# Performance work log

Measured on AMD Instinct MI355X. Metric: run time of the kernel, lower is better.

Reference implementation:

```python
import jax, jax.numpy as jnp
import numpy as np
import math

N_HEADS = 16
N_POINTS = 4
EPS = 1e-6


def layer_norm(x, g, b):
    m = x.mean(-1, keepdims=True)
    v = ((x - m) ** 2).mean(-1, keepdims=True)
    return (x - m) / jnp.sqrt(v + EPS) * g + b


def ref_points(H, W, dtype):
    # matches CrossSelfAtt.get_reference_points for one square level -> (1, H*W, 1, 2) in (x, y)
    ys = (jnp.arange(H, dtype=dtype) + 0.5) / H
    xs = (jnp.arange(W, dtype=dtype) + 0.5) / W
    gy, gx = jnp.meshgrid(ys, xs, indexing='ij')
    return jnp.stack([gx.reshape(-1), gy.reshape(-1)], -1)[None, :, None, :]


def bilinear(v, H, W, loc):
    # v: (B, H*W, nH, Dh); loc: (B, Lq, nH, P, 2) normalized [0,1]; zero padding, align_corners=False
    B, _, nH, Dh = v.shape
    Lq, P = loc.shape[1], loc.shape[3]
    x = loc[..., 0] * W - 0.5
    y = loc[..., 1] * H - 0.5
    x0 = jnp.floor(x)
    y0 = jnp.floor(y)
    wx1 = x - x0
    wy1 = y - y0
    x0i = x0.astype(jnp.int32)
    y0i = y0.astype(jnp.int32)
    vt = v.transpose(0, 2, 1, 3)  # (B, nH, HW, Dh)

    def corner(xi, yi, w):
        valid = (xi >= 0) & (xi < W) & (yi >= 0) & (yi < H)
        idx = jnp.clip(yi, 0, H - 1) * W + jnp.clip(xi, 0, W - 1)  # (B, Lq, nH, P)
        idx_t = idx.transpose(0, 2, 1, 3).reshape(B, nH, Lq * P)
        g = jnp.take_along_axis(vt, idx_t[..., None], axis=2).reshape(B, nH, Lq, P, Dh)
        return g.transpose(0, 2, 1, 3, 4) * (w * valid)[..., None]

    return (corner(x0i, y0i, (1 - wx1) * (1 - wy1))
            + corner(x0i + 1, y0i, wx1 * (1 - wy1))
            + corner(x0i, y0i + 1, (1 - wx1) * wy1)
            + corner(x0i + 1, y0i + 1, wx1 * wy1))


def msda(query, value_in, shapes, ref, Wv, bv, Woff, boff, Wa, ba, Wo, bo):
    # standard Deformable-DETR MSDeformAttn forward
    B, Lq, D = query.shape
    nH, P, L = N_HEADS, N_POINTS, len(shapes)
    Dh = D // nH
    value = (value_in @ Wv + bv).reshape(B, -1, nH, Dh)
    off = (query @ Woff + boff).reshape(B, Lq, nH, L, P, 2)
    aw = jax.nn.softmax((query @ Wa + ba).reshape(B, Lq, nH, L * P), -1).reshape(B, Lq, nH, L, P)
    norm = jnp.asarray([[w_, h_] for (h_, w_) in shapes], dtype=query.dtype)  # (L, 2) = (W, H)
    loc = ref[:, :, None, :, None, :] + off / norm[None, None, None, :, None, :]
    out = jnp.zeros((B, Lq, nH, Dh), query.dtype)
    start = 0
    for l, (H_, W_) in enumerate(shapes):
        samp = bilinear(value[:, start:start + H_ * W_], H_, W_, loc[:, :, :, l])
        out = out + (samp * aw[:, :, :, l, :, None]).sum(3)
        start += H_ * W_
    return out.reshape(B, Lq, D) @ Wo + bo


def setup_inputs() -> dict:
    key = jax.random.key(0)
    B, Lq, Lf, D = 2, 4096, 4096, 768
    nH, P, L = N_HEADS, N_POINTS, 1
    ks = jax.random.split(key, 20)
    w = lambda k, s: jax.random.normal(k, s, jnp.float32) * 0.02
    return {
        'query': jax.random.normal(ks[0], (B, Lq, D), jnp.float32),
        'feat': jax.random.normal(ks[1], (B, Lf, D), jnp.float32),
        'spatial_shapes': jnp.array([[64, 64]], jnp.int32),
        'level_start_index': jnp.array([0], jnp.int32),
        'qn_W': w(ks[2], (D, D)), 'qn_b': jnp.zeros((D,)), 'qn_g': jnp.ones((D,)), 'qn_beta': jnp.zeros((D,)),
        'fn_W': w(ks[3], (D, D)), 'fn_b': jnp.zeros((D,)), 'fn_g': jnp.ones((D,)), 'fn_beta': jnp.zeros((D,)),
        'nm_g': jnp.ones((D,)), 'nm_beta': jnp.zeros((D,)),
        'gamma1': jax.random.normal(ks[4], (D,), jnp.float32) * 0.1,
        'c_Wv': w(ks[5], (D, D)), 'c_bv': jnp.zeros((D,)),
        'c_Woff': w(ks[6], (D, nH * L * P * 2)),
        'c_boff': jax.random.uniform(ks[7], (nH * L * P * 2,), jnp.float32, -3.0, 3.0),
        'c_Wa': w(ks[8], (D, nH * L * P)), 'c_ba': jnp.zeros((nH * L * P,)),
        'c_Wo': w(ks[9], (D, D)), 'c_bo': jnp.zeros((D,)),
        's_Wv': w(ks[10], (D, D)), 's_bv': jnp.zeros((D,)),
        's_Woff': w(ks[11], (D, nH * L * P * 2)),
        's_boff': jax.random.uniform(ks[12], (nH * L * P * 2,), jnp.float32, -3.0, 3.0),
        's_Wa': w(ks[13], (D, nH * L * P)), 's_ba': jnp.zeros((nH * L * P,)),
        's_Wo': w(ks[14], (D, D)), 's_bo': jnp.zeros((D,)),
    }


def reference(query, feat, spatial_shapes, level_start_index, qn_W, qn_b, qn_g, qn_beta, fn_W, fn_b, fn_g, fn_beta, nm_g, nm_beta, gamma1, c_Wv, c_bv, c_Woff, c_boff, c_Wa, c_ba, c_Wo, c_bo, s_Wv, s_bv, s_Woff, s_boff, s_Wa, s_ba, s_Wo, s_bo):
    shapes = [(int(h), int(w_)) for h, w_ in np.asarray(spatial_shapes)]
    qe = int(math.sqrt(query.shape[1]))
    ref = ref_points(qe, qe, query.dtype)  # (1, Lq, 1, 2)
    qn = layer_norm(query @ qn_W + qn_b, qn_g, qn_beta)
    fn = layer_norm(feat @ fn_W + fn_b, fn_g, fn_beta)
    attn = msda(qn, fn, shapes, ref, c_Wv, c_bv, c_Woff, c_boff, c_Wa, c_ba, c_Wo, c_bo)
    attn1 = layer_norm(attn, nm_g, nm_beta)
    attn2 = msda(attn1, attn1, [(qe, qe)], ref, s_Wv, s_bv, s_Woff, s_boff, s_Wa, s_ba, s_Wo, s_bo)
    # note: source uses gamma1 for BOTH terms (gamma2 is unused)
    return attn * gamma1 + attn2 * gamma1
```

## Files before the change

kernel.cpp:

```cpp
#include <hip/hip_runtime.h>
#include <hip/hip_bf16.h>
#include <math.h>

#define D_MODEL 768
#define NH 16
#define DH 48
#define NP 4
#define LQ 4096
#define BB 2
#define MTOT (BB * LQ)

typedef __attribute__((ext_vector_type(8))) _Float16 half8_t;
typedef __attribute__((ext_vector_type(4))) float floatx4;

__device__ __forceinline__ void load_lds16(const void* g, void* l) {
    __builtin_amdgcn_global_load_lds((const __attribute__((address_space(1))) void*)g,
                                     (__attribute__((address_space(3))) void*)l, 16, 0, 0);
}

template <int MODE>
__device__ __forceinline__ void gemm_body(
    const _Float16* __restrict__ A, const _Float16* __restrict__ Wt,
    const float* __restrict__ bias, void* __restrict__ Cv, int ldc,
    int tm, int tn,
    const _Float16* __restrict__ attn, const float* __restrict__ gamma)
{
    constexpr int K = 768;
    constexpr int NT = K / 32;
    __shared__ _Float16 As[2][128 * 32];
    __shared__ _Float16 Bs[2][128 * 32];

    const int bm = tm * 128, bn = tn * 128;
    const int t = threadIdx.x;
    const int lane = t & 63;
    const int w = t >> 6;
    const int wm = (w >> 1) * 64, wn = (w & 1) * 64;

    floatx4 acc[4][4] = {};

    const int r0 = t >> 2;
    const int c8 = (t & 3) * 8;
    const size_t arow0 = (size_t)(bm + r0) * K + c8;
    const size_t arow1 = (size_t)(bm + 64 + r0) * K + c8;
    const size_t brow0 = (size_t)(bn + r0) * K + c8;
    const size_t brow1 = (size_t)(bn + 64 + r0) * K + c8;

    const int lrow = lane & 15;
    const int lk = (lane >> 4) * 8;

    load_lds16(A + arow0, &As[0][w * 512]);
    load_lds16(A + arow1, &As[0][2048 + w * 512]);
    load_lds16(Wt + brow0, &Bs[0][w * 512]);
    load_lds16(Wt + brow1, &Bs[0][2048 + w * 512]);
    __syncthreads();

    for (int ti = 0; ti < NT; ++ti) {
        const int cur = ti & 1;
        if (ti + 1 < NT) {
            const int kn = (ti + 1) * 32;
            const int nxt = cur ^ 1;
            load_lds16(A + arow0 + kn, &As[nxt][w * 512]);
            load_lds16(A + arow1 + kn, &As[nxt][2048 + w * 512]);
            load_lds16(Wt + brow0 + kn, &Bs[nxt][w * 512]);
            load_lds16(Wt + brow1 + kn, &Bs[nxt][2048 + w * 512]);
        }

        const _Float16* Ac = As[cur];
        const _Float16* Bc = Bs[cur];
        half8_t af[4], bf[4];
#pragma unroll
        for (int i = 0; i < 4; ++i) {
            af[i] = *(const half8_t*)&Ac[(wm + i * 16 + lrow) * 32 + lk];
            bf[i] = *(const half8_t*)&Bc[(wn + i * 16 + lrow) * 32 + lk];
        }
#pragma unroll
        for (int i = 0; i < 4; ++i)
#pragma unroll
            for (int j = 0; j < 4; ++j)
                acc[i][j] = __builtin_amdgcn_mfma_f32_16x16x32_f16(af[i], bf[j], acc[i][j], 0, 0, 0);

        if (ti + 1 < NT) __syncthreads();
    }

    const int rquad = (lane >> 4) * 4;
#pragma unroll
    for (int i = 0; i < 4; ++i) {
#pragma unroll
        for (int j = 0; j < 4; ++j) {
            const int col = bn + wn + j * 16 + lrow;
            const float bcol = bias[col];
#pragma unroll
            for (int r = 0; r < 4; ++r) {
                const size_t row = (size_t)(bm + wm + i * 16 + rquad + r);
                float v = acc[i][j][r] + bcol;
                if constexpr (MODE == 1) {
                    v = ((float)attn[row * (size_t)ldc + col] + v) * gamma[col];
                    ((float*)Cv)[row * (size_t)ldc + col] = v;
                } else if constexpr (MODE == 2) {
                    ((_Float16*)Cv)[row * (size_t)ldc + col] = (_Float16)v;
                } else {
                    ((float*)Cv)[row * (size_t)ldc + col] = v;
                }
            }
        }
    }
}

template <int MODE>
__global__ __launch_bounds__(256) void gemm_mfma(
    const _Float16* __restrict__ A, const _Float16* __restrict__ Wt,
    const float* __restrict__ bias, void* __restrict__ C,
    const _Float16* __restrict__ attn, const float* __restrict__ gamma)
{
    const int bid = blockIdx.x;
    const int swz = (bid & 7) * 48 + (bid >> 3);
    gemm_body<MODE>(A, Wt, bias, C, 768, swz & 63, swz >> 6, attn, gamma);
}

template <int M0, int M1>
__global__ __launch_bounds__(256) void dual_gemm(
    const _Float16* __restrict__ A0, const _Float16* __restrict__ W0,
    const float* __restrict__ b0, void* __restrict__ C0, int ldc0, int cnt0,
    const _Float16* __restrict__ A1, const _Float16* __restrict__ W1,
    const float* __restrict__ b1, void* __restrict__ C1, int ldc1, int cnt1)
{
    int bid = blockIdx.x;
    if (bid < cnt0) {
        const int q = cnt0 >> 3;
        const int swz = (bid & 7) * q + (bid >> 3);
        gemm_body<M0>(A0, W0, b0, C0, ldc0, swz & 63, swz >> 6, nullptr, nullptr);
    } else {
        bid -= cnt0;
        const int q = cnt1 >> 3;
        const int swz = (bid & 7) * q + (bid >> 3);
        gemm_body<M1>(A1, W1, b1, C1, ldc1, swz & 63, swz >> 6, nullptr, nullptr);
    }
}

__device__ __forceinline__ void ln_wave_body(
    const _Float16* __restrict__ X, _Float16* __restrict__ A,
    const float* __restrict__ g, const float* __restrict__ beta, int row)
{
    const int lane = threadIdx.x & 63;
    const _Float16* x = X + (size_t)row * D_MODEL;
    float v[12];
    float s = 0.f, s2 = 0.f;
#pragma unroll
    for (int j = 0; j < 12; ++j) {
        v[j] = (float)x[lane + 64 * j];
        s += v[j];
        s2 += v[j] * v[j];
    }
#pragma unroll
    for (int m = 1; m < 64; m <<= 1) {
        s += __shfl_xor(s, m);
        s2 += __shfl_xor(s2, m);
    }
    const float mean = s * (1.f / 768.f);
    const float var = s2 * (1.f / 768.f) - mean * mean;
    const float rstd = rsqrtf(var + 1e-6f);
    _Float16* arow = A + (size_t)row * D_MODEL;
#pragma unroll
    for (int j = 0; j < 12; ++j) {
        const int cc = lane + 64 * j;
        arow[cc] = (_Float16)((v[j] - mean) * rstd * g[cc] + beta[cc]);
    }
}

__global__ __launch_bounds__(256) void ln2_wave(
    const _Float16* __restrict__ X0, _Float16* __restrict__ A0,
    const float* __restrict__ g0, const float* __restrict__ b0,
    const _Float16* __restrict__ X1, _Float16* __restrict__ A1,
    const float* __restrict__ g1, const float* __restrict__ b1)
{
    const int r = blockIdx.x * 4 + (threadIdx.x >> 6);
    if (r < MTOT) ln_wave_body(X0, A0, g0, b0, r);
    else          ln_wave_body(X1, A1, g1, b1, r - MTOT);
}

__global__ __launch_bounds__(256) void ln_wave(
    const _Float16* __restrict__ X, _Float16* __restrict__ A,
    const float* __restrict__ g, const float* __restrict__ beta)
{
    const int r = blockIdx.x * 4 + (threadIdx.x >> 6);
    ln_wave_body(X, A, g, beta, r);
}

__global__ __launch_bounds__(256) void convert_all(
    const float* __restrict__ query, _Float16* __restrict__ actA,
    const float* __restrict__ feat, _Float16* __restrict__ actB,
    const float* __restrict__ w0, const float* __restrict__ w1,
    const float* __restrict__ w2, const float* __restrict__ w3,
    const float* __restrict__ w4, const float* __restrict__ w5,
    _Float16* __restrict__ Wall,
    const float* __restrict__ Woff_c, const float* __restrict__ Wa_c,
    const float* __restrict__ boff_c, const float* __restrict__ ba_c,
    const float* __restrict__ Woff_s, const float* __restrict__ Wa_s,
    const float* __restrict__ boff_s, const float* __restrict__ ba_s,
    _Float16* __restrict__ Wc, _Float16* __restrict__ Ws,
    float* __restrict__ bias_c, float* __restrict__ bias_s)
{
    __shared__ float tile[32][33];
    const int bid = blockIdx.x;
    const int t = threadIdx.x;

    if (bid < 12288) {
        const int i = bid * 256 + t;
        const int sel = i / (MTOT * 192);
        const int r = i - sel * (MTOT * 192);
        const float* X = sel ? feat : query;
        _Float16* D = sel ? actB : actA;
        const int c4 = r * 4;
        const float4 v = *(const float4*)(X + (size_t)c4);
        _Float16 o[4] = {(_Float16)v.x, (_Float16)v.y, (_Float16)v.z, (_Float16)v.w};
        *(uint2*)(D + (size_t)c4) = *(uint2*)o;
    } else if (bid < 15744) {
        const int g = bid - 12288;
        const int wi = g / 576;
        const int gx = g - wi * 576;
        const float* W = (wi == 0) ? w0 : (wi == 1) ? w1 : (wi == 2) ? w2
                       : (wi == 3) ? w3 : (wi == 4) ? w4 : w5;
        _Float16* Wt = Wall + (size_t)wi * 768 * 768;
        const int tk0 = (gx / 24) * 32;
        const int tn0 = (gx % 24) * 32;
#pragma unroll
        for (int r = 0; r < 4; ++r) {
            const int row = r * 8 + (t >> 5);
            const int col = t & 31;
            tile[row][col] = W[(size_t)(tk0 + row) * 768 + tn0 + col];
        }
        __syncthreads();
        const int n = t >> 3;
        const int kq = (t & 7) * 4;
        _Float16* dst = Wt + (size_t)(tn0 + n) * 768 + tk0 + kq;
#pragma unroll
        for (int u = 0; u < 4; ++u) dst[u] = (_Float16)tile[kq + u][n];
    } else {
        const int i = (bid - 15744) * 256 + t;
        if (i >= 2 * 256 * 192) return;
        const int pair = i / (256 * 192);
        const int r = i - pair * (256 * 192);
        const int n = r / 192;
        const int k0 = (r - n * 192) * 4;
        const float* Woff = pair ? Woff_s : Woff_c;
        const float* Wa = pair ? Wa_s : Wa_c;
        _Float16* dst = pair ? Ws : Wc;
        _Float16* row = dst + (size_t)n * 768;
#pragma unroll
        for (int u = 0; u < 4; ++u) {
            const int k = k0 + u;
            float v = (n < 128) ? Woff[(size_t)k * 128 + n]
                    : (n < 192) ? Wa[(size_t)k * 64 + (n - 128)] : 0.f;
            row[k] = (_Float16)v;
        }
        if (k0 == 0) {
            const float* boff = pair ? boff_s : boff_c;
            const float* ba = pair ? ba_s : ba_c;
            float* bias = pair ? bias_s : bias_c;
            bias[n] = (n < 128) ? boff[n] : (n < 192) ? ba[n - 128] : 0.f;
        }
    }
}

__global__ __launch_bounds__(192) void sample_fused(
    const _Float16* __restrict__ value, const float* __restrict__ offc,
    _Float16* __restrict__ A)
{
    __shared__ float loc_s[32][8];
    __shared__ float aw_s[32][4];

    const int bid = blockIdx.x;
    const int swz = (bid & 7) * 512 + (bid >> 3);
    const int bq_base = swz * 2;
    const int t = threadIdx.x;

    if (t < 32) {
        const int bq = bq_base + (t >> 4);
        const int h = t & 15;
        const int q = bq & (LQ - 1);
        const float* orow = offc + (size_t)bq * 256 + h * 8;
        const float* arow = offc + (size_t)bq * 256 + 128 + h * 4;
        float a0 = arow[0], a1 = arow[1], a2 = arow[2], a3 = arow[3];
        float mx = fmaxf(fmaxf(a0, a1), fmaxf(a2, a3));
        float e0 = expf(a0 - mx), e1 = expf(a1 - mx), e2 = expf(a2 - mx), e3 = expf(a3 - mx);
        float r = 1.f / (e0 + e1 + e2 + e3);
        const float refx = ((q & 63) + 0.5f) * (1.f / 64.f);
        const float refy = ((q >> 6) + 0.5f) * (1.f / 64.f);
#pragma unroll
        for (int p = 0; p < 4; ++p) {
            loc_s[t][p * 2 + 0] = refx + orow[p * 2 + 0] * (1.f / 64.f);
            loc_s[t][p * 2 + 1] = refy + orow[p * 2 + 1] * (1.f / 64.f);
        }
        aw_s[t][0] = e0 * r; aw_s[t][1] = e1 * r;
        aw_s[t][2] = e2 * r; aw_s[t][3] = e3 * r;
    }
    __syncthreads();

    const int lbqh = t / 6;
    const int c = t - lbqh * 6;
    const int d0 = c * 8;
    const int bq = bq_base + (lbqh >> 4);
    const int h = lbqh & 15;
    const int b = bq >> 12;

    const _Float16* vbase = value + (size_t)b * LQ * D_MODEL + h * DH + d0;

    float acc[8] = {};
#pragma unroll
    for (int p = 0; p < 4; ++p) {
        const float x = loc_s[lbqh][p * 2 + 0] * 64.f - 0.5f;
        const float y = loc_s[lbqh][p * 2 + 1] * 64.f - 0.5f;
        const float xf = floorf(x), yf = floorf(y);
        const float wx1 = x - xf, wy1 = y - yf;
        const float wx0 = 1.f - wx1, wy0 = 1.f - wy1;
        const int x0 = (int)xf, y0 = (int)yf;
        const int x1 = x0 + 1, y1 = y0 + 1;
        const float wp = aw_s[lbqh][p];
        const bool vx0 = (x0 >= 0) && (x0 < 64);
        const bool vx1 = (x1 >= 0) && (x1 < 64);
        const bool vy0 = (y0 >= 0) && (y0 < 64);
        const bool vy1 = (y1 >= 0) && (y1 < 64);
        const float cw[4] = {wp * wx0 * wy0, wp * wx1 * wy0, wp * wx0 * wy1, wp * wx1 * wy1};
        const bool cv[4] = {vx0 && vy0, vx1 && vy0, vx0 && vy1, vx1 && vy1};
        const int cxy[4][2] = {{x0, y0}, {x1, y0}, {x0, y1}, {x1, y1}};
#pragma unroll
        for (int k = 0; k < 4; ++k) {
            if (cv[k]) {
                const half8_t g = *(const half8_t*)(vbase + (size_t)(cxy[k][1] * 64 + cxy[k][0]) * D_MODEL);
#pragma unroll
                for (int u = 0; u < 8; ++u) acc[u] += cw[k] * (float)g[u];
            }
        }
    }

    _Float16* arow = A + (size_t)bq * D_MODEL + h * DH + d0;
    _Float16 o[8];
#pragma unroll
    for (int u = 0; u < 8; ++u) o[u] = (_Float16)acc[u];
    *(uint4*)arow = *(uint4*)o;
}

extern "C" void kernel_launch(void* const* d_in, const int* in_sizes, int n_in,
                              void* d_out, int out_size, void* d_ws, size_t ws_size,
                              hipStream_t stream)
{
    const float* query   = (const float*)d_in[0];
    const float* feat    = (const float*)d_in[1];
    const float* qn_W    = (const float*)d_in[4];
    const float* qn_b    = (const float*)d_in[5];
    const float* qn_g    = (const float*)d_in[6];
    const float* qn_beta = (const float*)d_in[7];
    const float* fn_W    = (const float*)d_in[8];
    const float* fn_b    = (const float*)d_in[9];
    const float* fn_g    = (const float*)d_in[10];
    const float* fn_beta = (const float*)d_in[11];
    const float* nm_g    = (const float*)d_in[12];
    const float* nm_beta = (const float*)d_in[13];
    const float* gamma1  = (const float*)d_in[14];
    const float* c_Wv    = (const float*)d_in[15];
    const float* c_bv    = (const float*)d_in[16];
    const float* c_Woff  = (const float*)d_in[17];
    const float* c_boff  = (const float*)d_in[18];
    const float* c_Wa    = (const float*)d_in[19];
    const float* c_ba    = (const float*)d_in[20];
    const float* c_Wo    = (const float*)d_in[21];
    const float* c_bo    = (const float*)d_in[22];
    const float* s_Wv    = (const float*)d_in[23];
    const float* s_bv    = (const float*)d_in[24];
    const float* s_Woff  = (const float*)d_in[25];
    const float* s_boff  = (const float*)d_in[26];
    const float* s_Wa    = (const float*)d_in[27];
    const float* s_ba    = (const float*)d_in[28];
    const float* s_Wo    = (const float*)d_in[29];
    const float* s_bo    = (const float*)d_in[30];

    const size_t SZ = (size_t)MTOT * D_MODEL;
    _Float16* hA    = (_Float16*)d_ws;
    _Float16* hB    = hA + SZ;
    _Float16* hQ    = hB + SZ;
    _Float16* hF    = hQ + SZ;
    _Float16* val16 = hF + SZ;
    float* offc   = (float*)(val16 + SZ);
    float* bias_c = offc + (size_t)MTOT * 256;
    float* bias_s = bias_c + 256;
    _Float16* W6 = (_Float16*)(bias_s + 256);
    _Float16* W_qn  = W6 + (size_t)0 * 768 * 768;
    _Float16* W_fn  = W6 + (size_t)1 * 768 * 768;
    _Float16* W_cWv = W6 + (size_t)2 * 768 * 768;
    _Float16* W_cWo = W6 + (size_t)3 * 768 * 768;
    _Float16* W_sWv = W6 + (size_t)4 * 768 * 768;
    _Float16* W_sWo = W6 + (size_t)5 * 768 * 768;
    _Float16* Woffa_c = W6 + (size_t)6 * 768 * 768;
    _Float16* Woffa_s = Woffa_c + (size_t)256 * 768;

    float* out = (float*)d_out;
    const dim3 blk(256);

    convert_all<<<16128, blk, 0, stream>>>(
        query, hA, feat, hB,
        qn_W, fn_W, c_Wv, c_Wo, s_Wv, s_Wo, W6,
        c_Woff, c_Wa, c_boff, c_ba, s_Woff, s_Wa, s_boff, s_ba,
        Woffa_c, Woffa_s, bias_c, bias_s);

    dual_gemm<2, 2><<<768, blk, 0, stream>>>(hA, W_qn, qn_b, hQ, 768, 384,
                                             hB, W_fn, fn_b, hF, 768, 384);
    ln2_wave<<<2 * MTOT / 4, blk, 0, stream>>>(hQ, hQ, qn_g, qn_beta,
                                               hF, hF, fn_g, fn_beta);
    dual_gemm<2, 0><<<512, blk, 0, stream>>>(hF, W_cWv, c_bv, val16, 768, 384,
                                             hQ, Woffa_c, bias_c, offc, 256, 128);
    sample_fused<<<4096, dim3(192), 0, stream>>>(val16, offc, hB);
    gemm_mfma<2><<<384, blk, 0, stream>>>(hB, W_cWo, c_bo, hA, nullptr, nullptr);

    ln_wave<<<MTOT / 4, blk, 0, stream>>>(hA, hQ, nm_g, nm_beta);
    dual_gemm<2, 0><<<512, blk, 0, stream>>>(hQ, W_sWv, s_bv, val16, 768, 384,
                                             hQ, Woffa_s, bias_s, offc, 256, 128);
    sample_fused<<<4096, dim3(192), 0, stream>>>(val16, offc, hB);
    gemm_mfma<1><<<384, blk, 0, stream>>>(hB, W_sWo, s_bo, out, hA, gamma1);
}
```

Baseline: 346.2 us.

## Fuse fp32 activation conversion into first GEMMs and store offsets as fp16

The first projection GEMMs now read fp32 query/feat directly, converting to fp16 in registers before the LDS store. This removes the separate activation conversion pass and its extra round trip through memory. The remaining weight transposes and these GEMMs are merged into one mega launch, with only the qn/fn weight transposes split into their own small kernel beforehand. The offset and attention-logit buffer is now fp16 instead of fp32, which halves that traffic at some cost in precision for the sampling locations. The fp32 A path uses register staging with a full vmcnt wait instead of async LDS loads, so loads may overlap less with compute.

Result: slower. 365.4 us (+5.5%).

```diff
diff --git a/kernel.cpp b/kernel.cpp
--- a/kernel.cpp
+++ b/kernel.cpp
@@ -18,9 +18,9 @@
                                      (__attribute__((address_space(3))) void*)l, 16, 0, 0);
 }
 
-template <int MODE>
+template <int MODE, bool AFP32>
 __device__ __forceinline__ void gemm_body(
-    const _Float16* __restrict__ A, const _Float16* __restrict__ Wt,
+    const void* __restrict__ Av, const _Float16* __restrict__ Wt,
     const float* __restrict__ bias, void* __restrict__ Cv, int ldc,
     int tm, int tn,
     const _Float16* __restrict__ attn, const float* __restrict__ gamma)
@@ -40,29 +40,60 @@
 
     const int r0 = t >> 2;
     const int c8 = (t & 3) * 8;
+    const size_t brow0 = (size_t)(bn + r0) * K + c8;
+    const size_t brow1 = (size_t)(bn + 64 + r0) * K + c8;
+
+    const int lrow = lane & 15;
+    const int lk = (lane >> 4) * 8;
+
+    const _Float16* A16 = (const _Float16*)Av;
+    const float* A32 = (const float*)Av;
     const size_t arow0 = (size_t)(bm + r0) * K + c8;
     const size_t arow1 = (size_t)(bm + 64 + r0) * K + c8;
-    const size_t brow0 = (size_t)(bn + r0) * K + c8;
-    const size_t brow1 = (size_t)(bn + 64 + r0) * K + c8;
-
-    const int lrow = lane & 15;
-    const int lk = (lane >> 4) * 8;
-
-    load_lds16(A + arow0, &As[0][w * 512]);
-    load_lds16(A + arow1, &As[0][2048 + w * 512]);
-    load_lds16(Wt + brow0, &Bs[0][w * 512]);
-    load_lds16(Wt + brow1, &Bs[0][2048 + w * 512]);
+
+    float4 ar[4];
+
+    auto STAGE_B = [&](int kt, int buf) {
+        load_lds16(Wt + brow0 + kt, &Bs[buf][w * 512]);
+        load_lds16(Wt + brow1 + kt, &Bs[buf][2048 + w * 512]);
+    };
+    auto STAGE_A16 = [&](int kt, int buf) {
+        load_lds16(A16 + arow0 + kt, &As[buf][w * 512]);
+        load_lds16(A16 + arow1 + kt, &As[buf][2048 + w * 512]);
+    };
+    auto LOAD_A32 = [&](int kt) {
+        const float* p0 = A32 + arow0 + kt;
+        const float* p1 = A32 + arow1 + kt;
+        ar[0] = *(const float4*)p0; ar[1] = *(const float4*)(p0 + 4);
+        ar[2] = *(const float4*)p1; ar[3] = *(const float4*)(p1 + 4);
+    };
+    auto WRITE_A32 = [&](int buf) {
+        _Float16 h0[8] = {(_Float16)ar[0].x, (_Float16)ar[0].y, (_Float16)ar[0].z, (_Float16)ar[0].w,
+                          (_Float16)ar[1].x, (_Float16)ar[1].y, (_Float16)ar[1].z, (_Float16)ar[1].w};
+        _Float16 h1[8] = {(_Float16)ar[2].x, (_Float16)ar[2].y, (_Float16)ar[2].z, (_Float16)ar[2].w,
+                          (_Float16)ar[3].x, (_Float16)ar[3].y, (_Float16)ar[3].z, (_Float16)ar[3].w};
+        *(half8_t*)&As[buf][r0 * 32 + c8] = *(half8_t*)h0;
+        *(half8_t*)&As[buf][2048 + r0 * 32 + c8] = *(half8_t*)h1;
+    };
+
+    STAGE_B(0, 0);
+    if constexpr (AFP32) {
+        LOAD_A32(0);
+        asm volatile("s_waitcnt vmcnt(0)" ::: "memory");
+        WRITE_A32(0);
+    } else {
+        STAGE_A16(0, 0);
+    }
     __syncthreads();
 
     for (int ti = 0; ti < NT; ++ti) {
         const int cur = ti & 1;
+        const int nxt = cur ^ 1;
         if (ti + 1 < NT) {
             const int kn = (ti + 1) * 32;
-            const int nxt = cur ^ 1;
-            load_lds16(A + arow0 + kn, &As[nxt][w * 512]);
-            load_lds16(A + arow1 + kn, &As[nxt][2048 + w * 512]);
-            load_lds16(Wt + brow0 + kn, &Bs[nxt][w * 512]);
-            load_lds16(Wt + brow1 + kn, &Bs[nxt][2048 + w * 512]);
+            STAGE_B(kn, nxt);
+            if constexpr (AFP32) LOAD_A32(kn);
+            else                 STAGE_A16(kn, nxt);
         }
 
         const _Float16* Ac = As[cur];
@@ -79,7 +110,13 @@
             for (int j = 0; j < 4; ++j)
                 acc[i][j] = __builtin_amdgcn_mfma_f32_16x16x32_f16(af[i], bf[j], acc[i][j], 0, 0, 0);
 
-        if (ti + 1 < NT) __syncthreads();
+        if (ti + 1 < NT) {
+            if constexpr (AFP32) {
+                asm volatile("s_waitcnt vmcnt(0)" ::: "memory");
+                WRITE_A32(nxt);
+            }
+            __syncthreads();
+        }
     }
 
     const int rquad = (lane >> 4) * 4;
@@ -96,100 +133,49 @@
                 if constexpr (MODE == 1) {
                     v = ((float)attn[row * (size_t)ldc + col] + v) * gamma[col];
                     ((float*)Cv)[row * (size_t)ldc + col] = v;
-                } else if constexpr (MODE == 2) {
+                } else {
                     ((_Float16*)Cv)[row * (size_t)ldc + col] = (_Float16)v;
-                } else {
-                    ((float*)Cv)[row * (size_t)ldc + col] = v;
                 }
             }
         }
     }
 }
 
-template <int MODE>
-__global__ __launch_bounds__(256) void gemm_mfma(
-    const _Float16* __restrict__ A, const _Float16* __restrict__ Wt,
-    const float* __restrict__ bias, void* __restrict__ C,
-    const _Float16* __restrict__ attn, const float* __restrict__ gamma)
-{
-    const int bid = blockIdx.x;
-    const int swz = (bid & 7) * 48 + (bid >> 3);
-    gemm_body<MODE>(A, Wt, bias, C, 768, swz & 63, swz >> 6, attn, gamma);
-}
-
-template <int M0, int M1>
-__global__ __launch_bounds__(256) void dual_gemm(
-    const _Float16* __restrict__ A0, const _Float16* __restrict__ W0,
-    const float* __restrict__ b0, void* __restrict__ C0, int ldc0, int cnt0,
-    const _Float16* __restrict__ A1, const _Float16* __restrict__ W1,
-    const float* __restrict__ b1, void* __restrict__ C1, int ldc1, int cnt1)
-{
-    int bid = blockIdx.x;
-    if (bid < cnt0) {
-        const int q = cnt0 >> 3;
-        const int swz = (bid & 7) * q + (bid >> 3);
-        gemm_body<M0>(A0, W0, b0, C0, ldc0, swz & 63, swz >> 6, nullptr, nullptr);
-    } else {
-        bid -= cnt0;
-        const int q = cnt1 >> 3;
-        const int swz = (bid & 7) * q + (bid >> 3);
-        gemm_body<M1>(A1, W1, b1, C1, ldc1, swz & 63, swz >> 6, nullptr, nullptr);
-    }
-}
-
-__device__ __forceinline__ void ln_wave_body(
-    const _Float16* __restrict__ X, _Float16* __restrict__ A,
-    const float* __restrict__ g, const float* __restrict__ beta, int row)
-{
-    const int lane = threadIdx.x & 63;
-    const _Float16* x = X + (size_t)row * D_MODEL;
-    float v[12];
-    float s = 0.f, s2 = 0.f;
-#pragma unroll
-    for (int j = 0; j < 12; ++j) {
-        v[j] = (float)x[lane + 64 * j];
-        s += v[j];
-        s2 += v[j] * v[j];
-    }
-#pragma unroll
-    for (int m = 1; m < 64; m <<= 1) {
-        s += __shfl_xor(s, m);
-        s2 += __shfl_xor(s2, m);
-    }
-    const float mean = s * (1.f / 768.f);
-    const float var = s2 * (1.f / 768.f) - mean * mean;
-    const float rstd = rsqrtf(var + 1e-6f);
-    _Float16* arow = A + (size_t)row * D_MODEL;
-#pragma unroll
-    for (int j = 0; j < 12; ++j) {
-        const int cc = lane + 64 * j;
-        arow[cc] = (_Float16)((v[j] - mean) * rstd * g[cc] + beta[cc]);
-    }
-}
-
-__global__ __launch_bounds__(256) void ln2_wave(
-    const _Float16* __restrict__ X0, _Float16* __restrict__ A0,
-    const float* __restrict__ g0, const float* __restrict__ b0,
-    const _Float16* __restrict__ X1, _Float16* __restrict__ A1,
-    const float* __restrict__ g1, const float* __restrict__ b1)
-{
-    const int r = blockIdx.x * 4 + (threadIdx.x >> 6);
-    if (r < MTOT) ln_wave_body(X0, A0, g0, b0, r);
-    else          ln_wave_body(X1, A1, g1, b1, r - MTOT);
-}
-
-__global__ __launch_bounds__(256) void ln_wave(
-    const _Float16* __restrict__ X, _Float16* __restrict__ A,
-    const float* __restrict__ g, const float* __restrict__ beta)
-{
-    const int r = blockIdx.x * 4 + (threadIdx.x >> 6);
-    ln_wave_body(X, A, g, beta, r);
-}
-
-__global__ __launch_bounds__(256) void convert_all(
-    const float* __restrict__ query, _Float16* __restrict__ actA,
-    const float* __restrict__ feat, _Float16* __restrict__ actB,
+__device__ __forceinline__ void wt_transpose_block(
+    const float* __restrict__ W, _Float16* __restrict__ Wt, int gx, int t,
+    float (*tile)[33])
+{
+    const int tk0 = (gx / 24) * 32;
+    const int tn0 = (gx % 24) * 32;
+#pragma unroll
+    for (int r = 0; r < 4; ++r) {
+        const int row = r * 8 + (t >> 5);
+        const int col = t & 31;
+        tile[row][col] = W[(size_t)(tk0 + row) * 768 + tn0 + col];
+    }
+    __syncthreads();
+    const int n = t >> 3;
+    const int kq = (t & 7) * 4;
+    _Float16* dst = Wt + (size_t)(tn0 + n) * 768 + tk0 + kq;
+#pragma unroll
+    for (int u = 0; u < 4; ++u) dst[u] = (_Float16)tile[kq + u][n];
+}
+
+__global__ __launch_bounds__(256) void convert_w2(
     const float* __restrict__ w0, const float* __restrict__ w1,
+    _Float16* __restrict__ Wall)
+{
+    __shared__ float tile[32][33];
+    const int wi = blockIdx.x / 576;
+    const int gx = blockIdx.x % 576;
+    wt_transpose_block(wi ? w1 : w0, Wall + (size_t)wi * 768 * 768, gx, threadIdx.x, tile);
+}
+
+__global__ __launch_bounds__(256) void g1_mega(
+    const float* __restrict__ query, const _Float16* __restrict__ Wq,
+    const float* __restrict__ bq_, _Float16* __restrict__ Cq,
+    const float* __restrict__ feat, const _Float16* __restrict__ Wf,
+    const float* __restrict__ bf_, _Float16* __restrict__ Cf,
     const float* __restrict__ w2, const float* __restrict__ w3,
     const float* __restrict__ w4, const float* __restrict__ w5,
     _Float16* __restrict__ Wall,
@@ -204,40 +190,21 @@
     const int bid = blockIdx.x;
     const int t = threadIdx.x;
 
-    if (bid < 12288) {
-        const int i = bid * 256 + t;
-        const int sel = i / (MTOT * 192);
-        const int r = i - sel * (MTOT * 192);
-        const float* X = sel ? feat : query;
-        _Float16* D = sel ? actB : actA;
-        const int c4 = r * 4;
-        const float4 v = *(const float4*)(X + (size_t)c4);
-        _Float16 o[4] = {(_Float16)v.x, (_Float16)v.y, (_Float16)v.z, (_Float16)v.w};
-        *(uint2*)(D + (size_t)c4) = *(uint2*)o;
-    } else if (bid < 15744) {
-        const int g = bid - 12288;
+    if (bid < 768) {
+        int b = (bid < 384) ? bid : bid - 384;
+        const int swz = (b & 7) * 48 + (b >> 3);
+        if (bid < 384)
+            gemm_body<2, true>(query, Wq, bq_, Cq, 768, swz & 63, swz >> 6, nullptr, nullptr);
+        else
+            gemm_body<2, true>(feat, Wf, bf_, Cf, 768, swz & 63, swz >> 6, nullptr, nullptr);
+    } else if (bid < 3072) {
+        const int g = bid - 768;
         const int wi = g / 576;
         const int gx = g - wi * 576;
-        const float* W = (wi == 0) ? w0 : (wi == 1) ? w1 : (wi == 2) ? w2
-                       : (wi == 3) ? w3 : (wi == 4) ? w4 : w5;
-        _Float16* Wt = Wall + (size_t)wi * 768 * 768;
-        const int tk0 = (gx / 24) * 32;
-        const int tn0 = (gx % 24) * 32;
-#pragma unroll
-        for (int r = 0; r < 4; ++r) {
-            const int row = r * 8 + (t >> 5);
-            const int col = t & 31;
-            tile[row][col] = W[(size_t)(tk0 + row) * 768 + tn0 + col];
-        }
-        __syncthreads();
-        const int n = t >> 3;
-        const int kq = (t & 7) * 4;
-        _Float16* dst = Wt + (size_t)(tn0 + n) * 768 + tk0 + kq;
-#pragma unroll
-        for (int u = 0; u < 4; ++u) dst[u] = (_Float16)tile[kq + u][n];
+        const float* W = (wi == 0) ? w2 : (wi == 1) ? w3 : (wi == 2) ? w4 : w5;
+        wt_transpose_block(W, Wall + (size_t)(wi + 2) * 768 * 768, gx, t, tile);
     } else {
-        const int i = (bid - 15744) * 256 + t;
-        if (i >= 2 * 256 * 192) return;
+        const int i = (bid - 3072) * 256 + t;
         const int pair = i / (256 * 192);
         const int r = i - pair * (256 * 192);
         const int n = r / 192;
@@ -262,8 +229,87 @@
     }
 }
 
+template <int MODE>
+__global__ __launch_bounds__(256) void gemm_mfma(
+    const _Float16* __restrict__ A, const _Float16* __restrict__ Wt,
+    const float* __restrict__ bias, void* __restrict__ C,
+    const _Float16* __restrict__ attn, const float* __restrict__ gamma)
+{
+    const int bid = blockIdx.x;
+    const int swz = (bid & 7) * 48 + (bid >> 3);
+    gemm_body<MODE, false>(A, Wt, bias, C, 768, swz & 63, swz >> 6, attn, gamma);
+}
+
+__global__ __launch_bounds__(256) void dual_gemm(
+    const _Float16* __restrict__ A0, const _Float16* __restrict__ W0,
+    const float* __restrict__ b0, void* __restrict__ C0, int ldc0, int cnt0,
+    const _Float16* __restrict__ A1, const _Float16* __restrict__ W1,
+    const float* __restrict__ b1, void* __restrict__ C1, int ldc1, int cnt1)
+{
+    int bid = blockIdx.x;
+    if (bid < cnt0) {
+        const int q = cnt0 >> 3;
+        const int swz = (bid & 7) * q + (bid >> 3);
+        gemm_body<2, false>(A0, W0, b0, C0, ldc0, swz & 63, swz >> 6, nullptr, nullptr);
+    } else {
+        bid -= cnt0;
+        const int q = cnt1 >> 3;
+        const int swz = (bid & 7) * q + (bid >> 3);
+        gemm_body<2, false>(A1, W1, b1, C1, ldc1, swz & 63, swz >> 6, nullptr, nullptr);
+    }
+}
+
+__device__ __forceinline__ void ln_wave_body(
+    const _Float16* __restrict__ X, _Float16* __restrict__ A,
+    const float* __restrict__ g, const float* __restrict__ beta, int row)
+{
+    const int lane = threadIdx.x & 63;
+    const _Float16* x = X + (size_t)row * D_MODEL;
+    float v[12];
+    float s = 0.f, s2 = 0.f;
+#pragma unroll
+    for (int j = 0; j < 12; ++j) {
+        v[j] = (float)x[lane + 64 * j];
+        s += v[j];
+        s2 += v[j] * v[j];
+    }
+#pragma unroll
+    for (int m = 1; m < 64; m <<= 1) {
+        s += __shfl_xor(s, m);
+        s2 += __shfl_xor(s2, m);
+    }
+    const float mean = s * (1.f / 768.f);
+    const float var = s2 * (1.f / 768.f) - mean * mean;
+    const float rstd = rsqrtf(var + 1e-6f);
+    _Float16* arow = A + (size_t)row * D_MODEL;
+#pragma unroll
+    for (int j = 0; j < 12; ++j) {
+        const int cc = lane + 64 * j;
+        arow[cc] = (_Float16)((v[j] - mean) * rstd * g[cc] + beta[cc]);
+    }
+}
+
+__global__ __launch_bounds__(256) void ln2_wave(
+    const _Float16* __restrict__ X0, _Float16* __restrict__ A0,
+    const float* __restrict__ g0, const float* __restrict__ b0,
+    const _Float16* __restrict__ X1, _Float16* __restrict__ A1,
+    const float* __restrict__ g1, const float* __restrict__ b1)
+{
+    const int r = blockIdx.x * 4 + (threadIdx.x >> 6);
+    if (r < MTOT) ln_wave_body(X0, A0, g0, b0, r);
+    else          ln_wave_body(X1, A1, g1, b1, r - MTOT);
+}
+
+__global__ __launch_bounds__(256) void ln_wave(
+    const _Float16* __restrict__ X, _Float16* __restrict__ A,
+    const float* __restrict__ g, const float* __restrict__ beta)
+{
+    const int r = blockIdx.x * 4 + (threadIdx.x >> 6);
+    ln_wave_body(X, A, g, beta, r);
+}
+
 __global__ __launch_bounds__(192) void sample_fused(
-    const _Float16* __restrict__ value, const float* __restrict__ offc,
+    const _Float16* __restrict__ value, const _Float16* __restrict__ offc,
     _Float16* __restrict__ A)
 {
     __shared__ float loc_s[32][8];
@@ -278,9 +324,9 @@
         const int bq = bq_base + (t >> 4);
         const int h = t & 15;
         const int q = bq & (LQ - 1);
-        const float* orow = offc + (size_t)bq * 256 + h * 8;
-        const float* arow = offc + (size_t)bq * 256 + 128 + h * 4;
-        float a0 = arow[0], a1 = arow[1], a2 = arow[2], a3 = arow[3];
+        const _Float16* orow = offc + (size_t)bq * 256 + h * 8;
+        const _Float16* arow = offc + (size_t)bq * 256 + 128 + h * 4;
+        float a0 = (float)arow[0], a1 = (float)arow[1], a2 = (float)arow[2], a3 = (float)arow[3];
         float mx = fmaxf(fmaxf(a0, a1), fmaxf(a2, a3));
         float e0 = expf(a0 - mx), e1 = expf(a1 - mx), e2 = expf(a2 - mx), e3 = expf(a3 - mx);
         float r = 1.f / (e0 + e1 + e2 + e3);
@@ -288,8 +334,8 @@
         const float refy = ((q >> 6) + 0.5f) * (1.f / 64.f);
 #pragma unroll
         for (int p = 0; p < 4; ++p) {
-            loc_s[t][p * 2 + 0] = refx + orow[p * 2 + 0] * (1.f / 64.f);
-            loc_s[t][p * 2 + 1] = refy + orow[p * 2 + 1] * (1.f / 64.f);
+            loc_s[t][p * 2 + 0] = refx + (float)orow[p * 2 + 0] * (1.f / 64.f);
+            loc_s[t][p * 2 + 1] = refy + (float)orow[p * 2 + 1] * (1.f / 64.f);
         }
         aw_s[t][0] = e0 * r; aw_s[t][1] = e1 * r;
         aw_s[t][2] = e2 * r; aw_s[t][3] = e3 * r;
@@ -380,8 +426,8 @@
     _Float16* hQ    = hB + SZ;
     _Float16* hF    = hQ + SZ;
     _Float16* val16 = hF + SZ;
-    float* offc   = (float*)(val16 + SZ);
-    float* bias_c = offc + (size_t)MTOT * 256;
+    _Float16* offc  = val16 + SZ;
+    float* bias_c = (float*)(offc + (size_t)MTOT * 256);
     float* bias_s = bias_c + 256;
     _Float16* W6 = (_Float16*)(bias_s + 256);
     _Float16* W_qn  = W6 + (size_t)0 * 768 * 768;
@@ -396,24 +442,25 @@
     float* out = (float*)d_out;
     const dim3 blk(256);
 
-    convert_all<<<16128, blk, 0, stream>>>(
-        query, hA, feat, hB,
-        qn_W, fn_W, c_Wv, c_Wo, s_Wv, s_Wo, W6,
+    convert_w2<<<1152, blk, 0, stream>>>(qn_W, fn_W, W6);
+
+    g1_mega<<<3456, blk, 0, stream>>>(
+        query, W_qn, qn_b, hQ,
+        feat, W_fn, fn_b, hF,
+        c_Wv, c_Wo, s_Wv, s_Wo, W6,
         c_Woff, c_Wa, c_boff, c_ba, s_Woff, s_Wa, s_boff, s_ba,
         Woffa_c, Woffa_s, bias_c, bias_s);
 
-    dual_gemm<2, 2><<<768, blk, 0, stream>>>(hA, W_qn, qn_b, hQ, 768, 384,
-                                             hB, W_fn, fn_b, hF, 768, 384);
     ln2_wave<<<2 * MTOT / 4, blk, 0, stream>>>(hQ, hQ, qn_g, qn_beta,
                                                hF, hF, fn_g, fn_beta);
-    dual_gemm<2, 0><<<512, blk, 0, stream>>>(hF, W_cWv, c_bv, val16, 768, 384,
-                                             hQ, Woffa_c, bias_c, offc, 256, 128);
+    dual_gemm<<<512, blk, 0, stream>>>(hF, W_cWv, c_bv, val16, 768, 384,
+                                       hQ, Woffa_c, bias_c, offc, 256, 128);
     sample_fused<<<4096, dim3(192), 0, stream>>>(val16, offc, hB);
     gemm_mfma<2><<<384, blk, 0, stream>>>(hB, W_cWo, c_bo, hA, nullptr, nullptr);
 
     ln_wave<<<MTOT / 4, blk, 0, stream>>>(hA, hQ, nm_g, nm_beta);
-    dual_gemm<2, 0><<<512, blk, 0, stream>>>(hQ, W_sWv, s_bv, val16, 768, 384,
-                                             hQ, Woffa_s, bias_s, offc, 256, 128);
+    dual_gemm<<<512, blk, 0, stream>>>(hQ, W_sWv, s_bv, val16, 768, 384,
+                                       hQ, Woffa_s, bias_s, offc, 256, 128);
     sample_fused<<<4096, dim3(192), 0, stream>>>(val16, offc, hB);
     gemm_mfma<1><<<384, blk, 0, stream>>>(hB, W_sWo, s_bo, out, hA, gamma1);
 }
```

## Overlap weight conversion with first GEMM pair and store offsets in fp16

Applied to the files above, without the earlier changes.

Splits the conversion kernel so that only the activations and the first two weights are converted up front. The remaining weight transposes and the offset/attention weight packing now run inside the first dual-GEMM launch as extra blocks, overlapping with the GEMM work and removing one launch. The offset/attention-logit projection output is also changed from fp32 to fp16, which halves that buffer's write and read traffic but lowers the precision of the sampling offsets and logits. Shared memory buffers are moved out of gemm_body so the fused kernel can reuse LDS as the transpose tile.

New measurement: 350.8 us. No clear change (+1.3%).

```diff
diff --git a/kernel.cpp b/kernel.cpp
--- a/kernel.cpp
+++ b/kernel.cpp
@@ -23,12 +23,11 @@
     const _Float16* __restrict__ A, const _Float16* __restrict__ Wt,
     const float* __restrict__ bias, void* __restrict__ Cv, int ldc,
     int tm, int tn,
-    const _Float16* __restrict__ attn, const float* __restrict__ gamma)
+    const _Float16* __restrict__ attn, const float* __restrict__ gamma,
+    _Float16* AsB, _Float16* BsB)
 {
     constexpr int K = 768;
     constexpr int NT = K / 32;
-    __shared__ _Float16 As[2][128 * 32];
-    __shared__ _Float16 Bs[2][128 * 32];
 
     const int bm = tm * 128, bn = tn * 128;
     const int t = threadIdx.x;
@@ -48,25 +47,24 @@
     const int lrow = lane & 15;
     const int lk = (lane >> 4) * 8;
 
-    load_lds16(A + arow0, &As[0][w * 512]);
-    load_lds16(A + arow1, &As[0][2048 + w * 512]);
-    load_lds16(Wt + brow0, &Bs[0][w * 512]);
-    load_lds16(Wt + brow1, &Bs[0][2048 + w * 512]);
+    auto STAGE = [&](int kt, int buf) {
+        _Float16* as = AsB + (buf << 12);
+        _Float16* bs = BsB + (buf << 12);
+        load_lds16(A + arow0 + kt, as + w * 512);
+        load_lds16(A + arow1 + kt, as + 2048 + w * 512);
+        load_lds16(Wt + brow0 + kt, bs + w * 512);
+        load_lds16(Wt + brow1 + kt, bs + 2048 + w * 512);
+    };
+
+    STAGE(0, 0);
     __syncthreads();
 
     for (int ti = 0; ti < NT; ++ti) {
         const int cur = ti & 1;
-        if (ti + 1 < NT) {
-            const int kn = (ti + 1) * 32;
-            const int nxt = cur ^ 1;
-            load_lds16(A + arow0 + kn, &As[nxt][w * 512]);
-            load_lds16(A + arow1 + kn, &As[nxt][2048 + w * 512]);
-            load_lds16(Wt + brow0 + kn, &Bs[nxt][w * 512]);
-            load_lds16(Wt + brow1 + kn, &Bs[nxt][2048 + w * 512]);
-        }
-
-        const _Float16* Ac = As[cur];
-        const _Float16* Bc = Bs[cur];
+        if (ti + 1 < NT) STAGE((ti + 1) * 32, cur ^ 1);
+
+        const _Float16* Ac = AsB + (cur << 12);
+        const _Float16* Bc = BsB + (cur << 12);
         half8_t af[4], bf[4];
 #pragma unroll
         for (int i = 0; i < 4; ++i) {
@@ -96,109 +94,39 @@
                 if constexpr (MODE == 1) {
                     v = ((float)attn[row * (size_t)ldc + col] + v) * gamma[col];
                     ((float*)Cv)[row * (size_t)ldc + col] = v;
-                } else if constexpr (MODE == 2) {
+                } else {
                     ((_Float16*)Cv)[row * (size_t)ldc + col] = (_Float16)v;
-                } else {
-                    ((float*)Cv)[row * (size_t)ldc + col] = v;
                 }
             }
         }
     }
 }
 
-template <int MODE>
-__global__ __launch_bounds__(256) void gemm_mfma(
-    const _Float16* __restrict__ A, const _Float16* __restrict__ Wt,
-    const float* __restrict__ bias, void* __restrict__ C,
-    const _Float16* __restrict__ attn, const float* __restrict__ gamma)
-{
-    const int bid = blockIdx.x;
-    const int swz = (bid & 7) * 48 + (bid >> 3);
-    gemm_body<MODE>(A, Wt, bias, C, 768, swz & 63, swz >> 6, attn, gamma);
-}
-
-template <int M0, int M1>
-__global__ __launch_bounds__(256) void dual_gemm(
-    const _Float16* __restrict__ A0, const _Float16* __restrict__ W0,
-    const float* __restrict__ b0, void* __restrict__ C0, int ldc0, int cnt0,
-    const _Float16* __restrict__ A1, const _Float16* __restrict__ W1,
-    const float* __restrict__ b1, void* __restrict__ C1, int ldc1, int cnt1)
-{
-    int bid = blockIdx.x;
-    if (bid < cnt0) {
-        const int q = cnt0 >> 3;
-        const int swz = (bid & 7) * q + (bid >> 3);
-        gemm_body<M0>(A0, W0, b0, C0, ldc0, swz & 63, swz >> 6, nullptr, nullptr);
-    } else {
-        bid -= cnt0;
-        const int q = cnt1 >> 3;
-        const int swz = (bid & 7) * q + (bid >> 3);
-        gemm_body<M1>(A1, W1, b1, C1, ldc1, swz & 63, swz >> 6, nullptr, nullptr);
-    }
-}
-
-__device__ __forceinline__ void ln_wave_body(
-    const _Float16* __restrict__ X, _Float16* __restrict__ A,
-    const float* __restrict__ g, const float* __restrict__ beta, int row)
-{
-    const int lane = threadIdx.x & 63;
-    const _Float16* x = X + (size_t)row * D_MODEL;
-    float v[12];
-    float s = 0.f, s2 = 0.f;
-#pragma unroll
-    for (int j = 0; j < 12; ++j) {
-        v[j] = (float)x[lane + 64 * j];
-        s += v[j];
-        s2 += v[j] * v[j];
-    }
-#pragma unroll
-    for (int m = 1; m < 64; m <<= 1) {
-        s += __shfl_xor(s, m);
-        s2 += __shfl_xor(s2, m);
-    }
-    const float mean = s * (1.f / 768.f);
-    const float var = s2 * (1.f / 768.f) - mean * mean;
-    const float rstd = rsqrtf(var + 1e-6f);
-    _Float16* arow = A + (size_t)row * D_MODEL;
-#pragma unroll
-    for (int j = 0; j < 12; ++j) {
-        const int cc = lane + 64 * j;
-        arow[cc] = (_Float16)((v[j] - mean) * rstd * g[cc] + beta[cc]);
-    }
-}
-
-__global__ __launch_bounds__(256) void ln2_wave(
-    const _Float16* __restrict__ X0, _Float16* __restrict__ A0,
-    const float* __restrict__ g0, const float* __restrict__ b0,
-    const _Float16* __restrict__ X1, _Float16* __restrict__ A1,
-    const float* __restrict__ g1, const float* __restrict__ b1)
-{
-    const int r = blockIdx.x * 4 + (threadIdx.x >> 6);
-    if (r < MTOT) ln_wave_body(X0, A0, g0, b0, r);
-    else          ln_wave_body(X1, A1, g1, b1, r - MTOT);
-}
-
-__global__ __launch_bounds__(256) void ln_wave(
-    const _Float16* __restrict__ X, _Float16* __restrict__ A,
-    const float* __restrict__ g, const float* __restrict__ beta)
-{
-    const int r = blockIdx.x * 4 + (threadIdx.x >> 6);
-    ln_wave_body(X, A, g, beta, r);
-}
-
-__global__ __launch_bounds__(256) void convert_all(
+__device__ __forceinline__ void wt_transpose_block(
+    const float* __restrict__ W, _Float16* __restrict__ Wt, int gx, int t,
+    float (*tile)[33])
+{
+    const int tk0 = (gx / 24) * 32;
+    const int tn0 = (gx % 24) * 32;
+#pragma unroll
+    for (int r = 0; r < 4; ++r) {
+        const int row = r * 8 + (t >> 5);
+        const int col = t & 31;
+        tile[row][col] = W[(size_t)(tk0 + row) * 768 + tn0 + col];
+    }
+    __syncthreads();
+    const int n = t >> 3;
+    const int kq = (t & 7) * 4;
+    _Float16* dst = Wt + (size_t)(tn0 + n) * 768 + tk0 + kq;
+#pragma unroll
+    for (int u = 0; u < 4; ++u) dst[u] = (_Float16)tile[kq + u][n];
+}
+
+__global__ __launch_bounds__(256) void convert_pre(
     const float* __restrict__ query, _Float16* __restrict__ actA,
     const float* __restrict__ feat, _Float16* __restrict__ actB,
     const float* __restrict__ w0, const float* __restrict__ w1,
-    const float* __restrict__ w2, const float* __restrict__ w3,
-    const float* __restrict__ w4, const float* __restrict__ w5,
-    _Float16* __restrict__ Wall,
-    const float* __restrict__ Woff_c, const float* __restrict__ Wa_c,
-    const float* __restrict__ boff_c, const float* __restrict__ ba_c,
-    const float* __restrict__ Woff_s, const float* __restrict__ Wa_s,
-    const float* __restrict__ boff_s, const float* __restrict__ ba_s,
-    _Float16* __restrict__ Wc, _Float16* __restrict__ Ws,
-    float* __restrict__ bias_c, float* __restrict__ bias_s)
+    _Float16* __restrict__ Wall)
 {
     __shared__ float tile[32][33];
     const int bid = blockIdx.x;
@@ -214,30 +142,50 @@
         const float4 v = *(const float4*)(X + (size_t)c4);
         _Float16 o[4] = {(_Float16)v.x, (_Float16)v.y, (_Float16)v.z, (_Float16)v.w};
         *(uint2*)(D + (size_t)c4) = *(uint2*)o;
-    } else if (bid < 15744) {
+    } else {
         const int g = bid - 12288;
         const int wi = g / 576;
         const int gx = g - wi * 576;
-        const float* W = (wi == 0) ? w0 : (wi == 1) ? w1 : (wi == 2) ? w2
-                       : (wi == 3) ? w3 : (wi == 4) ? w4 : w5;
-        _Float16* Wt = Wall + (size_t)wi * 768 * 768;
-        const int tk0 = (gx / 24) * 32;
-        const int tn0 = (gx % 24) * 32;
-#pragma unroll
-        for (int r = 0; r < 4; ++r) {
-            const int row = r * 8 + (t >> 5);
-            const int col = t & 31;
-            tile[row][col] = W[(size_t)(tk0 + row) * 768 + tn0 + col];
-        }
-        __syncthreads();
-        const int n = t >> 3;
-        const int kq = (t & 7) * 4;
-        _Float16* dst = Wt + (size_t)(tn0 + n) * 768 + tk0 + kq;
-#pragma unroll
-        for (int u = 0; u < 4; ++u) dst[u] = (_Float16)tile[kq + u][n];
+        wt_transpose_block(wi ? w1 : w0, Wall + (size_t)wi * 768 * 768, gx, t, tile);
+    }
+}
+
+__global__ __launch_bounds__(256) void g1_mega(
+    const _Float16* __restrict__ actA, const _Float16* __restrict__ Wq,
+    const float* __restrict__ bq_, _Float16* __restrict__ Cq,
+    const _Float16* __restrict__ actB, const _Float16* __restrict__ Wf,
+    const float* __restrict__ bf_, _Float16* __restrict__ Cf,
+    const float* __restrict__ w2, const float* __restrict__ w3,
+    const float* __restrict__ w4, const float* __restrict__ w5,
+    _Float16* __restrict__ Wall,
+    const float* __restrict__ Woff_c, const float* __restrict__ Wa_c,
+    const float* __restrict__ boff_c, const float* __restrict__ ba_c,
+    const float* __restrict__ Woff_s, const float* __restrict__ Wa_s,
+    const float* __restrict__ boff_s, const float* __restrict__ ba_s,
+    _Float16* __restrict__ Wc, _Float16* __restrict__ Ws,
+    float* __restrict__ bias_c, float* __restrict__ bias_s)
+{
+    __shared__ _Float16 AsS[2 * 4096];
+    __shared__ _Float16 BsS[2 * 4096];
+    const int bid = blockIdx.x;
+    const int t = threadIdx.x;
+
+    if (bid < 768) {
+        const int b = (bid < 384) ? bid : bid - 384;
+        const int swz = (b & 7) * 48 + (b >> 3);
+        if (bid < 384)
+            gemm_body<2>(actA, Wq, bq_, Cq, 768, swz & 63, swz >> 6, nullptr, nullptr, AsS, BsS);
+        else
+            gemm_body<2>(actB, Wf, bf_, Cf, 768, swz & 63, swz >> 6, nullptr, nullptr, AsS, BsS);
+    } else if (bid < 3072) {
+        float (*tile)[33] = reinterpret_cast<float (*)[33]>(AsS);
+        const int g = bid - 768;
+        const int wi = g / 576;
+        const int gx = g - wi * 576;
+        const float* W = (wi == 0) ? w2 : (wi == 1) ? w3 : (wi == 2) ? w4 : w5;
+        wt_transpose_block(W, Wall + (size_t)(wi + 2) * 768 * 768, gx, t, tile);
     } else {
-        const int i = (bid - 15744) * 256 + t;
-        if (i >= 2 * 256 * 192) return;
+        const int i = (bid - 3072) * 256 + t;
         const int pair = i / (256 * 192);
         const int r = i - pair * (256 * 192);
         const int n = r / 192;
@@ -262,8 +210,91 @@
     }
 }
 
+template <int MODE>
+__global__ __launch_bounds__(256) void gemm_mfma(
+    const _Float16* __restrict__ A, const _Float16* __restrict__ Wt,
+    const float* __restrict__ bias, void* __restrict__ C,
+    const _Float16* __restrict__ attn, const float* __restrict__ gamma)
+{
+    __shared__ _Float16 AsS[2 * 4096];
+    __shared__ _Float16 BsS[2 * 4096];
+    const int bid = blockIdx.x;
+    const int swz = (bid & 7) * 48 + (bid >> 3);
+    gemm_body<MODE>(A, Wt, bias, C, 768, swz & 63, swz >> 6, attn, gamma, AsS, BsS);
+}
+
+__global__ __launch_bounds__(256) void dual_gemm(
+    const _Float16* __restrict__ A0, const _Float16* __restrict__ W0,
+    const float* __restrict__ b0, _Float16* __restrict__ C0, int ldc0, int cnt0,
+    const _Float16* __restrict__ A1, const _Float16* __restrict__ W1,
+    const float* __restrict__ b1, _Float16* __restrict__ C1, int ldc1, int cnt1)
+{
+    __shared__ _Float16 AsS[2 * 4096];
+    __shared__ _Float16 BsS[2 * 4096];
+    int bid = blockIdx.x;
+    if (bid < cnt0) {
+        const int q = cnt0 >> 3;
+        const int swz = (bid & 7) * q + (bid >> 3);
+        gemm_body<2>(A0, W0, b0, C0, ldc0, swz & 63, swz >> 6, nullptr, nullptr, AsS, BsS);
+    } else {
+        bid -= cnt0;
+        const int q = cnt1 >> 3;
+        const int swz = (bid & 7) * q + (bid >> 3);
+        gemm_body<2>(A1, W1, b1, C1, ldc1, swz & 63, swz >> 6, nullptr, nullptr, AsS, BsS);
+    }
+}
+
+__device__ __forceinline__ void ln_wave_body(
+    const _Float16* __restrict__ X, _Float16* __restrict__ A,
+    const float* __restrict__ g, const float* __restrict__ beta, int row)
+{
+    const int lane = threadIdx.x & 63;
+    const _Float16* x = X + (size_t)row * D_MODEL;
+    float v[12];
+    float s = 0.f, s2 = 0.f;
+#pragma unroll
+    for (int j = 0; j < 12; ++j) {
+        v[j] = (float)x[lane + 64 * j];
+        s += v[j];
+        s2 += v[j] * v[j];
+    }
+#pragma unroll
+    for (int m = 1; m < 64; m <<= 1) {
+        s += __shfl_xor(s, m);
+        s2 += __shfl_xor(s2, m);
+    }
+    const float mean = s * (1.f / 768.f);
+    const float var = s2 * (1.f / 768.f) - mean * mean;
+    const float rstd = rsqrtf(var + 1e-6f);
+    _Float16* arow = A + (size_t)row * D_MODEL;
+#pragma unroll
+    for (int j = 0; j < 12; ++j) {
+        const int cc = lane + 64 * j;
+        arow[cc] = (_Float16)((v[j] - mean) * rstd * g[cc] + beta[cc]);
+    }
+}
+
+__global__ __launch_bounds__(256) void ln2_wave(
+    const _Float16* __restrict__ X0, _Float16* __restrict__ A0,
+    const float* __restrict__ g0, const float* __restrict__ b0,
+    const _Float16* __restrict__ X1, _Float16* __restrict__ A1,
+    const float* __restrict__ g1, const float* __restrict__ b1)
+{
+    const int r = blockIdx.x * 4 + (threadIdx.x >> 6);
+    if (r < MTOT) ln_wave_body(X0, A0, g0, b0, r);
+    else          ln_wave_body(X1, A1, g1, b1, r - MTOT);
+}
+
+__global__ __launch_bounds__(256) void ln_wave(
+    const _Float16* __restrict__ X, _Float16* __restrict__ A,
+    const float* __restrict__ g, const float* __restrict__ beta)
+{
+    const int r = blockIdx.x * 4 + (threadIdx.x >> 6);
+    ln_wave_body(X, A, g, beta, r);
+}
+
 __global__ __launch_bounds__(192) void sample_fused(
-    const _Float16* __restrict__ value, const float* __restrict__ offc,
+    const _Float16* __restrict__ value, const _Float16* __restrict__ offc,
     _Float16* __restrict__ A)
 {
     __shared__ float loc_s[32][8];
@@ -278,9 +309,9 @@
         const int bq = bq_base + (t >> 4);
         const int h = t & 15;
         const int q = bq & (LQ - 1);
-        const float* orow = offc + (size_t)bq * 256 + h * 8;
-        const float* arow = offc + (size_t)bq * 256 + 128 + h * 4;
-        float a0 = arow[0], a1 = arow[1], a2 = arow[2], a3 = arow[3];
+        const _Float16* orow = offc + (size_t)bq * 256 + h * 8;
+        const _Float16* arow = offc + (size_t)bq * 256 + 128 + h * 4;
+        float a0 = (float)arow[0], a1 = (float)arow[1], a2 = (float)arow[2], a3 = (float)arow[3];
         float mx = fmaxf(fmaxf(a0, a1), fmaxf(a2, a3));
         float e0 = expf(a0 - mx), e1 = expf(a1 - mx), e2 = expf(a2 - mx), e3 = expf(a3 - mx);
         float r = 1.f / (e0 + e1 + e2 + e3);
@@ -288,8 +319,8 @@
         const float refy = ((q >> 6) + 0.5f) * (1.f / 64.f);
 #pragma unroll
         for (int p = 0; p < 4; ++p) {
-            loc_s[t][p * 2 + 0] = refx + orow[p * 2 + 0] * (1.f / 64.f);
-            loc_s[t][p * 2 + 1] = refy + orow[p * 2 + 1] * (1.f / 64.f);
+            loc_s[t][p * 2 + 0] = refx + (float)orow[p * 2 + 0] * (1.f / 64.f);
+            loc_s[t][p * 2 + 1] = refy + (float)orow[p * 2 + 1] * (1.f / 64.f);
         }
         aw_s[t][0] = e0 * r; aw_s[t][1] = e1 * r;
         aw_s[t][2] = e2 * r; aw_s[t][3] = e3 * r;
@@ -380,8 +411,8 @@
     _Float16* hQ    = hB + SZ;
     _Float16* hF    = hQ + SZ;
     _Float16* val16 = hF + SZ;
-    float* offc   = (float*)(val16 + SZ);
-    float* bias_c = offc + (size_t)MTOT * 256;
+    _Float16* offc  = val16 + SZ;
+    float* bias_c = (float*)(offc + (size_t)MTOT * 256);
     float* bias_s = bias_c + 256;
     _Float16* W6 = (_Float16*)(bias_s + 256);
     _Float16* W_qn  = W6 + (size_t)0 * 768 * 768;
@@ -396,24 +427,25 @@
     float* out = (float*)d_out;
     const dim3 blk(256);
 
-    convert_all<<<16128, blk, 0, stream>>>(
-        query, hA, feat, hB,
-        qn_W, fn_W, c_Wv, c_Wo, s_Wv, s_Wo, W6,
+    convert_pre<<<13440, blk, 0, stream>>>(query, hA, feat, hB, qn_W, fn_W, W6);
+
+    g1_mega<<<3456, blk, 0, stream>>>(
+        hA, W_qn, qn_b, hQ,
+        hB, W_fn, fn_b, hF,
+        c_Wv, c_Wo, s_Wv, s_Wo, W6,
         c_Woff, c_Wa, c_boff, c_ba, s_Woff, s_Wa, s_boff, s_ba,
         Woffa_c, Woffa_s, bias_c, bias_s);
 
-    dual_gemm<2, 2><<<768, blk, 0, stream>>>(hA, W_qn, qn_b, hQ, 768, 384,
-                                             hB, W_fn, fn_b, hF, 768, 384);
     ln2_wave<<<2 * MTOT / 4, blk, 0, stream>>>(hQ, hQ, qn_g, qn_beta,
                                                hF, hF, fn_g, fn_beta);
-    dual_gemm<2, 0><<<512, blk, 0, stream>>>(hF, W_cWv, c_bv, val16, 768, 384,
-                                             hQ, Woffa_c, bias_c, offc, 256, 128);
+    dual_gemm<<<512, blk, 0, stream>>>(hF, W_cWv, c_bv, val16, 768, 384,
+                                       hQ, Woffa_c, bias_c, offc, 256, 128);
     sample_fused<<<4096, dim3(192), 0, stream>>>(val16, offc, hB);
     gemm_mfma<2><<<384, blk, 0, stream>>>(hB, W_cWo, c_bo, hA, nullptr, nullptr);
 
     ln_wave<<<MTOT / 4, blk, 0, stream>>>(hA, hQ, nm_g, nm_beta);
-    dual_gemm<2, 0><<<512, blk, 0, stream>>>(hQ, W_sWv, s_bv, val16, 768, 384,
-                                             hQ, Woffa_s, bias_s, offc, 256, 128);
+    dual_gemm<<<512, blk, 0, stream>>>(hQ, W_sWv, s_bv, val16, 768, 384,
+                                       hQ, Woffa_s, bias_s, offc, 256, 128);
     sample_fused<<<4096, dim3(192), 0, stream>>>(val16, offc, hB);
     gemm_mfma<1><<<384, blk, 0, stream>>>(hB, W_sWo, s_bo, out, hA, gamma1);
 }
```
